# Kernel tuning notes

Measured on AMD Instinct MI355X. Metric: run time of the kernel, lower is better.

## Reference

```python
import jax, jax.numpy as jnp
import numpy as np

N_NODES = 50000
N_EDGES = 800000
D = 128        # in_channels == out_channels
EDGE_DIM = 32
EPS = 0.0      # GINEConv default eps


def setup_inputs() -> dict:
    key = jax.random.key(0)
    ks = jax.random.split(key, 12)
    s = lambda d: 1.0 / np.sqrt(d)
    inp = {
        "x": jax.random.normal(ks[0], (N_NODES, D), jnp.float32),
        "edge_index": jax.random.randint(ks[1], (2, N_EDGES), 0, N_NODES, jnp.int64),
        "edge_attr": jax.random.normal(ks[2], (N_EDGES, EDGE_DIM), jnp.float32),
        "importance": jax.random.uniform(ks[3], (N_NODES, 1), jnp.float32),
        # GINEConv edge lin: Linear(edge_dim, in_channels)
        "We": jax.random.uniform(ks[4], (EDGE_DIM, D), jnp.float32, -s(EDGE_DIM), s(EDGE_DIM)),
        "be": jax.random.uniform(ks[5], (D,), jnp.float32, -s(EDGE_DIM), s(EDGE_DIM)),
        # GINEConv nn: Linear(in_channels, out_channels)
        "Wc": jax.random.uniform(ks[6], (D, D), jnp.float32, -s(D), s(D)),
        "bc": jax.random.uniform(ks[7], (D,), jnp.float32, -s(D), s(D)),
        # importance_gate: Linear(out_channels + 1, out_channels)
        "Wg": jax.random.uniform(ks[8], (D + 1, D), jnp.float32, -s(D + 1), s(D + 1)),
        "bg": jax.random.uniform(ks[9], (D,), jnp.float32, -s(D + 1), s(D + 1)),
        # importance_propagation: Linear(out_channels, 1)
        "Wp": jax.random.uniform(ks[10], (D, 1), jnp.float32, -s(D), s(D)),
        "bp": jax.random.uniform(ks[11], (1,), jnp.float32, -s(D), s(D)),
    }
    return inp


def reference(x, edge_index, edge_attr, importance, We, be, Wc, bc, Wg, bg, Wp, bp):
    src, dst = edge_index[0], edge_index[1]
    # GINEConv: messages = relu(x_j + lin(edge_attr)), aggregated by sum at dst
    e = edge_attr @ We + be                      # [E, D]
    msg = jax.nn.relu(x[src] + e)                # [E, D] gather + fused add/relu
    agg = jax.ops.segment_sum(msg, dst, num_segments=N_NODES)  # [N, D] scatter-add
    conv_out = ((1.0 + EPS) * x + agg) @ Wc + bc  # [N, D]
    # importance gating + residual
    gate_in = jnp.concatenate([conv_out, importance], axis=-1)  # [N, D+1]
    gate = jax.nn.sigmoid(gate_in @ Wg + bg)
    out = gate * conv_out + (1.0 - gate) * x
    propagated_importance = out @ Wp + bp        # [N, 1]
    return (out, propagated_importance)
```

## Files before the change

kernel.cpp:

```cpp
#include <hip/hip_runtime.h>

#define NN 50000
#define NE 800000
#define DD 128
#define ED 32
#define NB 196

typedef short  bf16x8 __attribute__((ext_vector_type(8)));
typedef float  f32x4  __attribute__((ext_vector_type(4)));
typedef float  f32x16 __attribute__((ext_vector_type(16)));

__device__ __forceinline__ float4 ld4(const float* p) {
    return *reinterpret_cast<const float4*>(p);
}
__device__ __forceinline__ short f2bf(float f) {
    unsigned u = __float_as_uint(f);
    u += 0x7fffu + ((u >> 16) & 1u);
    return (short)(u >> 16);
}
__device__ __forceinline__ int sniff64(const int* ei) {
    return ((ei[1] | ei[3] | ei[5] | ei[7]) == 0) ? 1 : 0;
}

__global__ __launch_bounds__(256)
void k_setup(const float* __restrict__ x, const int* __restrict__ ei,
             const float* __restrict__ We, unsigned int* __restrict__ xb,
             int* __restrict__ counts, unsigned short* __restrict__ Bft)
{
    const int tid = threadIdx.x;
    if (blockIdx.x < 6250) {
        const int t = blockIdx.x * 256 + tid;
        if (t >= NN * 32) return;
        const int n = t >> 5, c = t & 31;
        const float* xr = x + (size_t)n * DD + c;
        const unsigned b0 = (unsigned short)f2bf(xr[0]);
        const unsigned b1 = (unsigned short)f2bf(xr[32]);
        const unsigned b2 = (unsigned short)f2bf(xr[64]);
        const unsigned b3 = (unsigned short)f2bf(xr[96]);
        xb[(size_t)n * 64 + c * 2]     = b0 | (b1 << 16);
        xb[(size_t)n * 64 + c * 2 + 1] = b2 | (b3 << 16);
    } else if (blockIdx.x < 8298) {
        const int is64 = sniff64(ei);
        const int2* ei2 = (const int2*)ei;
        for (int e = (blockIdx.x - 6250) * 256 + tid; e < NE; e += 2048 * 256) {
            const int dst = is64 ? ei2[NE + e].x : ei[NE + e];
            atomicAdd(&counts[dst], 1);
        }
    } else if (tid < 64) {
        const int col = tid & 31, h = tid >> 5;
#pragma unroll
        for (int bb = 0; bb < 4; ++bb)
#pragma unroll
            for (int s = 0; s < 2; ++s)
#pragma unroll
                for (int i = 0; i < 8; ++i)
                    Bft[tid * 64 + (bb * 2 + s) * 8 + i] =
                        (unsigned short)f2bf(We[(s * 16 + h * 8 + i) * DD + bb * 32 + col]);
    }
}

__global__ __launch_bounds__(256)
void k_bsum(const int* __restrict__ counts, int* __restrict__ bsum) {
    const int i = blockIdx.x * 256 + threadIdx.x;
    int c = (i < NN) ? counts[i] : 0;
#pragma unroll
    for (int off = 32; off; off >>= 1) c += __shfl_xor(c, off, 64);
    __shared__ int ws4[4];
    if ((threadIdx.x & 63) == 0) ws4[threadIdx.x >> 6] = c;
    __syncthreads();
    if (threadIdx.x == 0) bsum[blockIdx.x] = ws4[0] + ws4[1] + ws4[2] + ws4[3];
}

__global__ __launch_bounds__(256)
void k_scanb(const int* __restrict__ bsum, int* __restrict__ bexcl) {
    const int tid = threadIdx.x, lane = tid & 63, w = tid >> 6;
    const int v = (tid < NB) ? bsum[tid] : 0;
    int s = v;
#pragma unroll
    for (int off = 1; off < 64; off <<= 1) {
        const int t = __shfl_up(s, off, 64);
        if (lane >= off) s += t;
    }
    __shared__ int wsum[4], wexcl[4];
    if (lane == 63) wsum[w] = s;
    __syncthreads();
    if (tid == 0) {
        int r = 0;
#pragma unroll
        for (int k = 0; k < 4; ++k) { wexcl[k] = r; r += wsum[k]; }
    }
    __syncthreads();
    if (tid < NB) bexcl[tid] = wexcl[w] + s - v;
}

__global__ __launch_bounds__(256)
void k_rowptr(const int* __restrict__ counts, const int* __restrict__ bexcl,
              int* __restrict__ cursor) {
    const int tid = threadIdx.x, lane = tid & 63, w = tid >> 6;
    const int i = blockIdx.x * 256 + tid;
    const int c = (i < NN) ? counts[i] : 0;
    int s = c;
#pragma unroll
    for (int off = 1; off < 64; off <<= 1) {
        const int t = __shfl_up(s, off, 64);
        if (lane >= off) s += t;
    }
    __shared__ int wsum[4], wexcl[4];
    if (lane == 63) wsum[w] = s;
    __syncthreads();
    if (tid == 0) {
        int r = 0;
#pragma unroll
        for (int k = 0; k < 4; ++k) { wexcl[k] = r; r += wsum[k]; }
    }
    __syncthreads();
    if (i < NN) cursor[i] = bexcl[blockIdx.x] + wexcl[w] + s - c;
}

__global__ __launch_bounds__(256)
void k_scatter2(const int* __restrict__ ei, int* __restrict__ cursor,
                const float* __restrict__ ea, int* __restrict__ sdat4,
                unsigned int* __restrict__ ebs)
{
    const int tid = threadIdx.x;
    const int e0  = blockIdx.x * 128;
    __shared__ int spos[128];
    if (tid < 128) {
        const int is64 = sniff64(ei);
        const int2* ei2 = (const int2*)ei;
        const int e   = e0 + tid;
        const int src = is64 ? ei2[e].x : ei[e];
        const int dst = is64 ? ei2[NE + e].x : ei[NE + e];
        const int pos = atomicAdd(&cursor[dst], 1);
        sdat4[pos] = src | (dst << 16);
        spos[tid] = pos;
    }
    __syncthreads();
#pragma unroll
    for (int it = 0; it < 8; ++it) {
        const int task = it * 256 + tid;
        const int el   = task >> 4;
        const int part = task & 15;
        const float2 v = *reinterpret_cast<const float2*>(
                             ea + (size_t)(e0 + el) * ED + part * 2);
        const unsigned lo = (unsigned short)f2bf(v.x);
        const unsigned hi = (unsigned short)f2bf(v.y);
        ebs[(size_t)spos[el] * 16 + part] = lo | (hi << 16);
    }
}

__device__ __forceinline__ void agg_epilogue(f32x16 (&C)[4], const float beb[4],
                                             int dstv, int lane, int col, int h,
                                             float* __restrict__ agg)
{
#pragma unroll
    for (int bb = 0; bb < 4; ++bb)
#pragma unroll
        for (int reg = 0; reg < 16; ++reg)
            C[bb][reg] = fmaxf(C[bb][reg] + beb[bb], 0.0f);

    const int  prv  = __shfl(dstv, (lane == 0) ? 0 : lane - 1, 64);
    const bool flag = (lane < 32) && ((col == 0) || (dstv != prv));
    unsigned rem = (unsigned)(__ballot(flag) & 0xFFFFFFFFull);

    while (rem) {
        const int ms = __ffs((int)rem) - 1;
        rem &= rem - 1;
        const int hi = rem ? (__ffs((int)rem) - 1) : 32;
        const int d  = __shfl(dstv, ms, 64);

        float v0 = 0.f, v1 = 0.f, v2 = 0.f, v3 = 0.f;
#pragma unroll
        for (int reg = 0; reg < 16; ++reg) {
            const int E = (reg & 3) + 8 * (reg >> 2) + 4 * h;
            const float mk = (E >= ms && E < hi) ? 1.0f : 0.0f;
            v0 = fmaf(mk, C[0][reg], v0);
            v1 = fmaf(mk, C[1][reg], v1);
            v2 = fmaf(mk, C[2][reg], v2);
            v3 = fmaf(mk, C[3][reg], v3);
        }
        v0 += __shfl_xor(v0, 32, 64);
        v1 += __shfl_xor(v1, 32, 64);
        v2 += __shfl_xor(v2, 32, 64);
        v3 += __shfl_xor(v3, 32, 64);

        float* ar = agg + (size_t)d * DD + h * 64 + col;
        unsafeAtomicAdd(ar,      h ? v2 : v0);
        unsafeAtomicAdd(ar + 32, h ? v3 : v1);
    }
}

__global__ __launch_bounds__(256, 2)
void k_aggE(const unsigned int* __restrict__ xb, const unsigned int* __restrict__ ebs,
            const unsigned short* __restrict__ Bft, const float* __restrict__ be,
            const int* __restrict__ sdat4, float* __restrict__ agg)
{
    const int lane = threadIdx.x & 63;
    const int col  = lane & 31;
    const int h    = lane >> 5;
    const int wid  = (blockIdx.x << 2) | (threadIdx.x >> 6);
    const int c0   = wid * 2, c1 = wid * 2 + 1;

    bf16x8 Bf[4][2];
    {
        const bf16x8* bp_ = reinterpret_cast<const bf16x8*>(Bft + lane * 64);
#pragma unroll
        for (int bb = 0; bb < 4; ++bb) {
            Bf[bb][0] = bp_[bb * 2];
            Bf[bb][1] = bp_[bb * 2 + 1];
        }
    }
    float beb[4];
#pragma unroll
    for (int bb = 0; bb < 4; ++bb) beb[bb] = be[bb * 32 + col];

    const int sd0 = sdat4[c0 * 32 + col];
    const int sd1 = sdat4[c1 * 32 + col];

    const unsigned int* ebr0 = ebs + ((size_t)c0 * 32 + col) * 16;
    const unsigned int* ebr1 = ebs + ((size_t)c1 * 32 + col) * 16;
    const bf16x8 A00 = *reinterpret_cast<const bf16x8*>(ebr0 + h * 4);
    const bf16x8 A01 = *reinterpret_cast<const bf16x8*>(ebr0 + 8 + h * 4);
    const bf16x8 A10 = *reinterpret_cast<const bf16x8*>(ebr1 + h * 4);
    const bf16x8 A11 = *reinterpret_cast<const bf16x8*>(ebr1 + 8 + h * 4);

    uint2 w0[16];
#pragma unroll
    for (int reg = 0; reg < 16; ++reg) {
        const int E   = (reg & 3) + 8 * (reg >> 2) + 4 * h;
        const int src = __shfl(sd0, E, 64) & 0xFFFF;
        w0[reg] = *reinterpret_cast<const uint2*>(xb + (size_t)src * 64 + col * 2);
    }

    f32x16 C[4];
#pragma unroll
    for (int reg = 0; reg < 16; ++reg) {
        C[0][reg] = __uint_as_float(w0[reg].x << 16);
        C[1][reg] = __uint_as_float(w0[reg].x & 0xFFFF0000u);
        C[2][reg] = __uint_as_float(w0[reg].y << 16);
        C[3][reg] = __uint_as_float(w0[reg].y & 0xFFFF0000u);
    }
#pragma unroll
    for (int bb = 0; bb < 4; ++bb) {
        C[bb] = __builtin_amdgcn_mfma_f32_32x32x16_bf16(A00, Bf[bb][0], C[bb], 0, 0, 0);
        C[bb] = __builtin_amdgcn_mfma_f32_32x32x16_bf16(A01, Bf[bb][1], C[bb], 0, 0, 0);
    }

    uint2 w1[16];
#pragma unroll
    for (int reg = 0; reg < 16; ++reg) {
        const int E   = (reg & 3) + 8 * (reg >> 2) + 4 * h;
        const int src = __shfl(sd1, E, 64) & 0xFFFF;
        w1[reg] = *reinterpret_cast<const uint2*>(xb + (size_t)src * 64 + col * 2);
    }

    agg_epilogue(C, beb, ((unsigned)sd0) >> 16, lane, col, h, agg);

#pragma unroll
    for (int reg = 0; reg < 16; ++reg) {
        C[0][reg] = __uint_as_float(w1[reg].x << 16);
        C[1][reg] = __uint_as_float(w1[reg].x & 0xFFFF0000u);
        C[2][reg] = __uint_as_float(w1[reg].y << 16);
        C[3][reg] = __uint_as_float(w1[reg].y & 0xFFFF0000u);
    }
#pragma unroll
    for (int bb = 0; bb < 4; ++bb) {
        C[bb] = __builtin_amdgcn_mfma_f32_32x32x16_bf16(A10, Bf[bb][0], C[bb], 0, 0, 0);
        C[bb] = __builtin_amdgcn_mfma_f32_32x32x16_bf16(A11, Bf[bb][1], C[bb], 0, 0, 0);
    }
    agg_epilogue(C, beb, ((unsigned)sd1) >> 16, lane, col, h, agg);
}

__global__ __launch_bounds__(256)
void k_cg(const float* __restrict__ x, const float* agg,
          const float* __restrict__ Wc, const float* __restrict__ bc,
          const float* __restrict__ imp, const float* __restrict__ Wg,
          const float* __restrict__ bg, const float* __restrict__ Wp,
          const float* __restrict__ bp, float* outp, float* __restrict__ prop)
{
    __shared__ short sBh[2048 * 8];
    __shared__ short sBl[2048 * 8];
    for (int idx = threadIdx.x; idx < 2048; idx += 256) {
        const int kk = idx >> 9;
        const int b  = (idx >> 6) & 7;
        const int l  = idx & 63;
        const int row0 = kk * 32 + ((l >> 4) << 3);
        const int col  = b * 16 + (l & 15);
        bf16x8 h8;
#pragma unroll
        for (int j = 0; j < 8; ++j)
            h8[j] = f2bf(Wc[(row0 + j) * DD + col]);
        *reinterpret_cast<bf16x8*>(&sBh[idx * 8]) = h8;
    }
    __syncthreads();

    const int lane = threadIdx.x & 63;
    const int ncol = lane & 15;
    const int krow = (lane >> 4) << 3;
    const int grp  = lane >> 4;
    const int wib  = threadIdx.x >> 6;
    const int wid  = (blockIdx.x << 2) | wib;
    const bool live = (wid < NN / 16);
    const int m0 = live ? wid * 16 : 0;

    f32x4 C[8];
#pragma unroll
    for (int b = 0; b < 8; ++b) {
        const float bcv = bc[b * 16 + ncol];
        f32x4 c = { bcv, bcv, bcv, bcv };
        C[b] = c;
    }
    {
        const float* xrow = x   + (size_t)(m0 + ncol) * DD + krow;
        const float* grow = agg + (size_t)(m0 + ncol) * DD + krow;
#pragma unroll
        for (int kk = 0; kk < 4; ++kk) {
            const float4 x0 = ld4(xrow + kk * 32), x1 = ld4(xrow + kk * 32 + 4);
            const float4 g0 = ld4(grow + kk * 32), g1 = ld4(grow + kk * 32 + 4);
            const float av[8] = { x0.x + g0.x, x0.y + g0.y, x0.z + g0.z, x0.w + g0.w,
                                  x1.x + g1.x, x1.y + g1.y, x1.z + g1.z, x1.w + g1.w };
            bf16x8 Ah;
#pragma unroll
            for (int j = 0; j < 8; ++j) Ah[j] = f2bf(av[j]);
#pragma unroll
            for (int b = 0; b < 8; ++b) {
                const bf16x8 Bh = *reinterpret_cast<const bf16x8*>(&sBh[((kk * 8 + b) * 64 + lane) * 8]);
                C[b] = __builtin_amdgcn_mfma_f32_16x16x32_bf16(Ah, Bh, C[b], 0, 0, 0);
            }
        }
    }
    __syncthreads();

    for (int idx = threadIdx.x; idx < 2048; idx += 256) {
        const int kk = idx >> 9;
        const int b  = (idx >> 6) & 7;
        const int l  = idx & 63;
        const int row0 = kk * 32 + ((l >> 4) << 3);
        const int col  = b * 16 + (l & 15);
        bf16x8 h8;
#pragma unroll
        for (int j = 0; j < 8; ++j)
            h8[j] = f2bf(Wg[(row0 + j) * DD + col]);
        *reinterpret_cast<bf16x8*>(&sBh[idx * 8]) = h8;
    }
    float* scr = reinterpret_cast<float*>(sBl) + wib * 2048;
#pragma unroll
    for (int r = 0; r < 4; ++r)
#pragma unroll
        for (int b = 0; b < 8; ++b)
            scr[(grp * 4 + r) * DD + b * 16 + ncol] = C[b][r];
    __syncthreads();

    f32x4 Z[8];
#pragma unroll
    for (int b = 0; b < 8; ++b) {
        const float bgv = bg[b * 16 + ncol];
        f32x4 z = { bgv, bgv, bgv, bgv };
        Z[b] = z;
    }
#pragma unroll
    for (int kk = 0; kk < 4; ++kk) {
        const float4 a0 = ld4(scr + ncol * DD + kk * 32 + krow);
        const float4 a1 = ld4(scr + ncol * DD + kk * 32 + krow + 4);
        const float av[8] = { a0.x, a0.y, a0.z, a0.w, a1.x, a1.y, a1.z, a1.w };
        bf16x8 Ah;
#pragma unroll
        for (int j = 0; j < 8; ++j) Ah[j] = f2bf(av[j]);
#pragma unroll
        for (int b = 0; b < 8; ++b) {
            const bf16x8 Bh = *reinterpret_cast<const bf16x8*>(&sBh[((kk * 8 + b) * 64 + lane) * 8]);
            Z[b] = __builtin_amdgcn_mfma_f32_16x16x32_bf16(Ah, Bh, Z[b], 0, 0, 0);
        }
    }

    if (!live) return;

    float wgi[8], wp8[8];
#pragma unroll
    for (int b = 0; b < 8; ++b) {
        wgi[b] = Wg[DD * DD + b * 16 + ncol];
        wp8[b] = Wp[b * 16 + ncol];
    }
    const float bps = bp[0];

    float s[4] = { 0.f, 0.f, 0.f, 0.f };
#pragma unroll
    for (int r = 0; r < 4; ++r) {
        const int m = m0 + grp * 4 + r;
        const float im = imp[m];
        const float* xr = x + (size_t)m * DD + ncol;
        float* orow = outp + (size_t)m * DD + ncol;
#pragma unroll
        for (int b = 0; b < 8; ++b) {
            const float a = Z[b][r] + im * wgi[b];
            const float g = 1.0f / (1.0f + expf(-a));
            const float xv = xr[b * 16];
            const float o = fmaf(g, C[b][r] - xv, xv);
            orow[b * 16] = o;
            s[r] += o * wp8[b];
        }
    }
#pragma unroll
    for (int off = 1; off < 16; off <<= 1) {
        s[0] += __shfl_xor(s[0], off, 64);
        s[1] += __shfl_xor(s[1], off, 64);
        s[2] += __shfl_xor(s[2], off, 64);
        s[3] += __shfl_xor(s[3], off, 64);
    }
    if (ncol < 4) {
        const float v = (ncol == 0) ? s[0] : (ncol == 1) ? s[1] : (ncol == 2) ? s[2] : s[3];
        prop[m0 + grp * 4 + ncol] = v + bps;
    }
}

extern "C" void kernel_launch(void* const* d_in, const int* in_sizes, int n_in,
                              void* d_out, int out_size, void* d_ws, size_t ws_size,
                              hipStream_t stream) {
    const float* x   = (const float*)d_in[0];
    const int*   ei  = (const int*)d_in[1];
    const float* ea  = (const float*)d_in[2];
    const float* imp = (const float*)d_in[3];
    const float* We  = (const float*)d_in[4];
    const float* be  = (const float*)d_in[5];
    const float* Wc  = (const float*)d_in[6];
    const float* bc  = (const float*)d_in[7];
    const float* Wg  = (const float*)d_in[8];
    const float* bg  = (const float*)d_in[9];
    const float* Wp  = (const float*)d_in[10];
    const float* bp  = (const float*)d_in[11];

    float* out  = (float*)d_out;
    float* prop = out + (size_t)NN * DD;
    float* agg  = out;

    int*            counts = (int*)d_ws;
    int*            cursor = (int*)((char*)d_ws + 204800);
    int*            bsum   = (int*)((char*)d_ws + 409600);
    int*            bexcl  = (int*)((char*)d_ws + 413696);
    unsigned short* Bft    = (unsigned short*)((char*)d_ws + 417792);
    int*            sdat4  = (int*)((char*)d_ws + 1048576);
    unsigned int*   xb     = (unsigned int*)((char*)d_ws + 4456448);
    unsigned int*   ebs    = (unsigned int*)((char*)d_ws + 17301504);

    hipMemsetAsync(counts, 0, NN * sizeof(int), stream);
    hipMemsetAsync(agg, 0, (size_t)NN * DD * sizeof(float), stream);
    hipLaunchKernelGGL(k_setup,    dim3(8299), dim3(256), 0, stream,
                       x, ei, We, xb, counts, Bft);
    hipLaunchKernelGGL(k_bsum,     dim3(NB),   dim3(256), 0, stream, counts, bsum);
    hipLaunchKernelGGL(k_scanb,    dim3(1),    dim3(256), 0, stream, bsum, bexcl);
    hipLaunchKernelGGL(k_rowptr,   dim3(NB),   dim3(256), 0, stream, counts, bexcl, cursor);
    hipLaunchKernelGGL(k_scatter2, dim3(6250), dim3(256), 0, stream, ei, cursor, ea, sdat4, ebs);
    hipLaunchKernelGGL(k_aggE,     dim3(3125), dim3(256), 0, stream,
                       xb, ebs, Bft, be, sdat4, agg);
    hipLaunchKernelGGL(k_cg,       dim3(782),  dim3(256), 0, stream,
                       x, agg, Wc, bc, imp, Wg, bg, Wp, bp, out, prop);
}
```

Baseline: 205.3 us.

## Fuse three scan kernels into one with spin-wait global sync and agg zeroing

Merges the block-sum, top-level scan and row-pointer kernels into a single launch. Blocks coordinate through global atomic flags and spin-waits, so the grid must be fully co-resident or it can deadlock. The zeroing of agg is folded into extra blocks of the same kernel, replacing a separate memset. The memset now clears counts and the sync flags together. In the scatter kernel, edge_attr loads are issued before the atomic cursor reservation to overlap their latency.

Result: slower. 212.9 us (+3.7%).

```diff
diff --git a/kernel.cpp b/kernel.cpp
--- a/kernel.cpp
+++ b/kernel.cpp
@@ -5,6 +5,7 @@
 #define DD 128
 #define ED 32
 #define NB 196
+#define NZB 1563
 
 typedef short  bf16x8 __attribute__((ext_vector_type(8)));
 typedef float  f32x4  __attribute__((ext_vector_type(4)));
@@ -60,61 +61,71 @@
 }
 
 __global__ __launch_bounds__(256)
-void k_bsum(const int* __restrict__ counts, int* __restrict__ bsum) {
-    const int i = blockIdx.x * 256 + threadIdx.x;
-    int c = (i < NN) ? counts[i] : 0;
-#pragma unroll
-    for (int off = 32; off; off >>= 1) c += __shfl_xor(c, off, 64);
-    __shared__ int ws4[4];
-    if ((threadIdx.x & 63) == 0) ws4[threadIdx.x >> 6] = c;
-    __syncthreads();
-    if (threadIdx.x == 0) bsum[blockIdx.x] = ws4[0] + ws4[1] + ws4[2] + ws4[3];
-}
-
-__global__ __launch_bounds__(256)
-void k_scanb(const int* __restrict__ bsum, int* __restrict__ bexcl) {
+void k_scan3(const int* __restrict__ counts, int* __restrict__ cursor,
+             int* __restrict__ bsum, int* __restrict__ bexcl,
+             int* __restrict__ syncf, float* __restrict__ aggz)
+{
     const int tid = threadIdx.x, lane = tid & 63, w = tid >> 6;
-    const int v = (tid < NB) ? bsum[tid] : 0;
-    int s = v;
+    const int bid = blockIdx.x;
+
+    if (bid >= NB) {
+        const int base = ((bid - NB) * 256 + tid) * 16;
+        if (base < NN * DD) {
+            const float4 z = { 0.f, 0.f, 0.f, 0.f };
+            float4* p = reinterpret_cast<float4*>(aggz + base);
+            p[0] = z; p[1] = z; p[2] = z; p[3] = z;
+        }
+        return;
+    }
+
+    __shared__ int wsum[4], wexcl1[4], wsum2[4], wexcl2[4];
+
+    const int i = bid * 256 + tid;
+    const int c = (i < NN) ? counts[i] : 0;
+    int s = c;
 #pragma unroll
     for (int off = 1; off < 64; off <<= 1) {
         const int t = __shfl_up(s, off, 64);
         if (lane >= off) s += t;
     }
-    __shared__ int wsum[4], wexcl[4];
     if (lane == 63) wsum[w] = s;
     __syncthreads();
     if (tid == 0) {
+        atomicExch(&bsum[bid], wsum[0] + wsum[1] + wsum[2] + wsum[3]);
+        __threadfence();
+        atomicAdd(&syncf[0], 1);
         int r = 0;
 #pragma unroll
-        for (int k = 0; k < 4; ++k) { wexcl[k] = r; r += wsum[k]; }
-    }
-    __syncthreads();
-    if (tid < NB) bexcl[tid] = wexcl[w] + s - v;
-}
-
-__global__ __launch_bounds__(256)
-void k_rowptr(const int* __restrict__ counts, const int* __restrict__ bexcl,
-              int* __restrict__ cursor) {
-    const int tid = threadIdx.x, lane = tid & 63, w = tid >> 6;
-    const int i = blockIdx.x * 256 + tid;
-    const int c = (i < NN) ? counts[i] : 0;
-    int s = c;
-#pragma unroll
-    for (int off = 1; off < 64; off <<= 1) {
-        const int t = __shfl_up(s, off, 64);
-        if (lane >= off) s += t;
-    }
-    __shared__ int wsum[4], wexcl[4];
-    if (lane == 63) wsum[w] = s;
-    __syncthreads();
-    if (tid == 0) {
-        int r = 0;
-#pragma unroll
-        for (int k = 0; k < 4; ++k) { wexcl[k] = r; r += wsum[k]; }
-    }
-    __syncthreads();
-    if (i < NN) cursor[i] = bexcl[blockIdx.x] + wexcl[w] + s - c;
+        for (int k = 0; k < 4; ++k) { wexcl1[k] = r; r += wsum[k]; }
+    }
+
+    if (bid == 0) {
+        if (tid == 0) { while (atomicAdd(&syncf[0], 0) < NB) { } }
+        __syncthreads();
+        const int v = (tid < NB) ? atomicAdd(&bsum[tid], 0) : 0;
+        int s2 = v;
+#pragma unroll
+        for (int off = 1; off < 64; off <<= 1) {
+            const int t = __shfl_up(s2, off, 64);
+            if (lane >= off) s2 += t;
+        }
+        if (lane == 63) wsum2[w] = s2;
+        __syncthreads();
+        if (tid == 0) {
+            int r = 0;
+#pragma unroll
+            for (int k = 0; k < 4; ++k) { wexcl2[k] = r; r += wsum2[k]; }
+        }
+        __syncthreads();
+        if (tid < NB) atomicExch(&bexcl[tid], wexcl2[w] + s2 - v);
+        __threadfence();
+        if (tid == 0) atomicExch(&syncf[1], 1);
+    }
+
+    if (tid == 0) { while (atomicAdd(&syncf[1], 0) == 0) { } }
+    __syncthreads();
+    const int be_ = atomicAdd(&bexcl[bid], 0);
+    if (i < NN) cursor[i] = be_ + wexcl1[w] + s - c;
 }
 
 __global__ __launch_bounds__(256)
@@ -124,6 +135,17 @@
 {
     const int tid = threadIdx.x;
     const int e0  = blockIdx.x * 128;
+
+    float2 v[8];
+#pragma unroll
+    for (int it = 0; it < 8; ++it) {
+        const int task = it * 256 + tid;
+        const int el   = task >> 4;
+        const int part = task & 15;
+        v[it] = *reinterpret_cast<const float2*>(
+                    ea + (size_t)(e0 + el) * ED + part * 2);
+    }
+
     __shared__ int spos[128];
     if (tid < 128) {
         const int is64 = sniff64(ei);
@@ -141,10 +163,8 @@
         const int task = it * 256 + tid;
         const int el   = task >> 4;
         const int part = task & 15;
-        const float2 v = *reinterpret_cast<const float2*>(
-                             ea + (size_t)(e0 + el) * ED + part * 2);
-        const unsigned lo = (unsigned short)f2bf(v.x);
-        const unsigned hi = (unsigned short)f2bf(v.y);
+        const unsigned lo = (unsigned short)f2bf(v[it].x);
+        const unsigned hi = (unsigned short)f2bf(v[it].y);
         ebs[(size_t)spos[el] * 16 + part] = lo | (hi << 16);
     }
 }
@@ -434,6 +454,7 @@
     float* agg  = out;
 
     int*            counts = (int*)d_ws;
+    int*            syncf  = (int*)((char*)d_ws + 200000);
     int*            cursor = (int*)((char*)d_ws + 204800);
     int*            bsum   = (int*)((char*)d_ws + 409600);
     int*            bexcl  = (int*)((char*)d_ws + 413696);
@@ -442,16 +463,15 @@
     unsigned int*   xb     = (unsigned int*)((char*)d_ws + 4456448);
     unsigned int*   ebs    = (unsigned int*)((char*)d_ws + 17301504);
 
-    hipMemsetAsync(counts, 0, NN * sizeof(int), stream);
-    hipMemsetAsync(agg, 0, (size_t)NN * DD * sizeof(float), stream);
-    hipLaunchKernelGGL(k_setup,    dim3(8299), dim3(256), 0, stream,
+    hipMemsetAsync(d_ws, 0, 200064, stream);
+    hipLaunchKernelGGL(k_setup,    dim3(8299),     dim3(256), 0, stream,
                        x, ei, We, xb, counts, Bft);
-    hipLaunchKernelGGL(k_bsum,     dim3(NB),   dim3(256), 0, stream, counts, bsum);
-    hipLaunchKernelGGL(k_scanb,    dim3(1),    dim3(256), 0, stream, bsum, bexcl);
-    hipLaunchKernelGGL(k_rowptr,   dim3(NB),   dim3(256), 0, stream, counts, bexcl, cursor);
-    hipLaunchKernelGGL(k_scatter2, dim3(6250), dim3(256), 0, stream, ei, cursor, ea, sdat4, ebs);
-    hipLaunchKernelGGL(k_aggE,     dim3(3125), dim3(256), 0, stream,
+    hipLaunchKernelGGL(k_scan3,    dim3(NB + NZB), dim3(256), 0, stream,
+                       counts, cursor, bsum, bexcl, syncf, agg);
+    hipLaunchKernelGGL(k_scatter2, dim3(6250),     dim3(256), 0, stream,
+                       ei, cursor, ea, sdat4, ebs);
+    hipLaunchKernelGGL(k_aggE,     dim3(3125),     dim3(256), 0, stream,
                        xb, ebs, Bft, be, sdat4, agg);
-    hipLaunchKernelGGL(k_cg,       dim3(782),  dim3(256), 0, stream,
+    hipLaunchKernelGGL(k_cg,       dim3(782),      dim3(256), 0, stream,
                        x, agg, Wc, bc, imp, Wg, bg, Wp, bp, out, prop);
 }
```
